# Kernel optimization log

Measured on AMD Instinct MI355X. Metric: run time of the kernel, lower is better.

The kernel has to match this reference:

```python
import jax, jax.numpy as jnp
import numpy as np

# Model dims (match init_kwargs)
NUM_INPUT_FEATURES = 100000
NUM_LABELS = 262144
EMBED_DIM = 256
H, DH = 4, 64          # num_heads, head_dim (EMBED_DIM = H*DH)
R, M = 2, 32           # num_quadrature_nodes, SLAY num_features
B, S = 4096, 64        # batch, history length
TOTAL_LABELS = 20480   # flattened ragged positive labels (~5/sample)
EPS = 1e-6
C = 2.0 + EPS

_nodes, _weights = np.polynomial.laguerre.laggauss(R)
QUAD_NODES = jnp.asarray(_nodes, dtype=jnp.float32) / C
QUAD_WEIGHTS = jnp.asarray(_weights, dtype=jnp.float32) / C


def slay_features(x, omega):
    """SLAY feature map. x: [N, EMBED_DIM] -> [N, H*R*M]."""
    n = x.shape[0]
    xr = x.reshape(n, H, DH)
    norm = jnp.linalg.norm(xr, axis=-1, keepdims=True)
    xn = xr / jnp.maximum(norm, 1e-6)                      # safe_normalize
    proj = jnp.einsum('bhd,rhdm->rbhm', xn, omega)         # [R,N,H,M]
    inv_sqrt_m = 1.0 / jnp.sqrt(jnp.float32(M))
    poly = (proj * proj) * inv_sqrt_m
    s = QUAD_NODES.reshape(-1, 1, 1, 1)
    sqrt_2s = jnp.sqrt(2.0 * jnp.maximum(s, 0.0))
    prf = jnp.exp(jnp.clip(proj * sqrt_2s - s, -10.0, 10.0)) * inv_sqrt_m
    w = jnp.sqrt(jnp.maximum(QUAD_WEIGHTS.reshape(-1, 1, 1, 1), 0.0))
    fused = poly * prf * w                                 # [R,N,H,M]
    return fused.transpose(1, 2, 0, 3).reshape(n, -1)      # [N, H*R*M]


def setup_inputs() -> dict:
    key = jax.random.key(0)
    k1, k2, k3, k4, k5 = jax.random.split(key, 5)
    indices = jax.random.randint(k1, (B, S), 0, NUM_INPUT_FEATURES, dtype=jnp.int64)
    mask = jnp.ones((B, S), dtype=jnp.float32)
    flat_labels = jax.random.randint(k2, (TOTAL_LABELS,), 0, NUM_LABELS, dtype=jnp.int64)
    sample_ids = jnp.sort(jax.random.randint(k3, (TOTAL_LABELS,), 0, B, dtype=jnp.int64))
    embed_table = jax.random.normal(k4, (NUM_INPUT_FEATURES, EMBED_DIM), dtype=jnp.float32)
    kw, ko = jax.random.split(k5)
    W_vecs = jax.random.normal(kw, (NUM_LABELS, EMBED_DIM), dtype=jnp.float32) / jnp.sqrt(jnp.float32(EMBED_DIM))
    omega = jax.random.normal(ko, (R, H, DH, M), dtype=jnp.float32)
    return {"indices": indices, "mask": mask, "flat_labels": flat_labels,
            "sample_ids": sample_ids, "embed_table": embed_table,
            "W_vecs": W_vecs, "omega": omega}


def reference(indices, mask, flat_labels, sample_ids, embed_table, W_vecs, omega):
    # MeanEmbedding encoder
    embeds = embed_table[indices]                                   # [B,S,D]
    sum_emb = jnp.sum(embeds * mask[:, :, None], axis=1)
    query = sum_emb / jnp.maximum(jnp.sum(mask, axis=1, keepdims=True), 1e-9)
    phi_q = slay_features(query, omega)                             # [B,F]
    phi_W = slay_features(W_vecs, omega)                            # [L,F]
    Z_vec = jnp.sum(phi_W, axis=0)                                  # [F]
    log_Z = jnp.log(phi_q @ Z_vec + 1e-6)                           # [B]
    # ragged positive-label terms, flattened (same math as per-sample loop)
    nums = jnp.sum(phi_W[flat_labels] * phi_q[sample_ids], axis=-1) + 1e-6
    loss_total = -jnp.sum(jnp.log(nums) - log_Z[sample_ids])
    return loss_total / B
```

## Files before the change

kernel.cpp:

```cpp
#include <hip/hip_runtime.h>
#include <hip/hip_bf16.h>
#include <math.h>

#define BB 4096
#define SS 64
#define DD 256
#define NH 4
#define DH 64
#define MM 32
#define NLAB 262144
#define TLAB 20480
#define ISM 0.17677669529663687f

typedef __attribute__((ext_vector_type(8))) short short8;
typedef __attribute__((ext_vector_type(4))) float f32x4;

static __device__ __forceinline__ short f2bf(float f) {
    __hip_bfloat16 h = __float2bfloat16(f);
    return *reinterpret_cast<short*>(&h);
}

__global__ __launch_bounds__(256) void k_query_phi(
    const int* __restrict__ idx, const float* __restrict__ mask,
    const float* __restrict__ emb, const float* __restrict__ omega,
    float* __restrict__ phiq, float* __restrict__ Zvec,
    float s0f, float s1f, float q0f, float q1f, float cw0, float cw1)
{
    const int b = blockIdx.x, t = threadIdx.x;
    const int h = t >> 6, r = (t >> 5) & 1, m = t & 31;
    if (b == 0) Zvec[t] = 0.0f;

    __shared__ int   lidx[SS];
    __shared__ float lmk[SS];
    if (t < SS) { lidx[t] = idx[b * SS + t]; lmk[t] = mask[b * SS + t]; }

    float omg[DH];
    const float* ob = omega + (size_t)((r * NH + h) * DH) * MM + m;
#pragma unroll
    for (int d = 0; d < DH; ++d) omg[d] = ob[d * MM];

    __syncthreads();

    float acc = 0.0f, msum = 0.0f;
#pragma unroll 8
    for (int s = 0; s < SS; ++s) {
        int   id = lidx[s];
        float mv = lmk[s];
        acc   = fmaf(emb[(size_t)id * DD + t], mv, acc);
        msum += mv;
    }
    float q = acc / fmaxf(msum, 1e-9f);

    float ss = q * q;
#pragma unroll
    for (int off = 32; off >= 1; off >>= 1) ss += __shfl_xor(ss, off);
    float xn = q / fmaxf(sqrtf(ss), 1e-6f);

    __shared__ float lxn[DD];
    lxn[t] = xn;
    __syncthreads();

    float p = 0.0f;
    const float* xb = lxn + h * DH;
#pragma unroll
    for (int d = 0; d < DH; ++d) p = fmaf(xb[d], omg[d], p);

    const float sv = r ? s1f : s0f, qv = r ? q1f : q0f, cw = r ? cw1 : cw0;
    float arg = fminf(fmaxf(fmaf(p, qv, -sv), -10.0f), 10.0f);
    phiq[b * DD + t] = p * p * __expf(arg) * cw;
}

__global__ __launch_bounds__(256) void k_zvec(
    const float* __restrict__ W, const float* __restrict__ omega,
    float* __restrict__ Zvec, int lab_per_block,
    float s0f, float s1f, float q0f, float q1f, float cw0, float cw1)
{
    const int t = threadIdx.x;
    const int h    = t >> 6;
    const int lane = t & 63;
    const int l15  = lane & 15;
    const int kg   = lane >> 4;

    short8 bf[4][2];
#pragma unroll
    for (int nt = 0; nt < 4; ++nt) {
        const int r = nt >> 1;
        const int m = (nt & 1) * 16 + l15;
        const float* ob = omega + (size_t)((r * NH + h) * DH) * MM + m;
#pragma unroll
        for (int kh = 0; kh < 2; ++kh)
#pragma unroll
            for (int e = 0; e < 8; ++e) {
                int d = kh * 32 + kg * 8 + e;
                bf[nt][kh][e] = f2bf(ob[(size_t)d * MM]);
            }
    }

    float zp[4] = {0.0f, 0.0f, 0.0f, 0.0f};
    const int l0 = blockIdx.x * lab_per_block;

    for (int tile = 0; tile < lab_per_block; tile += 16) {
        const float* wp = W + (size_t)(l0 + tile + l15) * DD + h * DH + kg * 8;
        float4 f0 = *(const float4*)(wp);
        float4 f1 = *(const float4*)(wp + 4);
        float4 f2 = *(const float4*)(wp + 32);
        float4 f3 = *(const float4*)(wp + 36);

        float ss = f0.x*f0.x + f0.y*f0.y + f0.z*f0.z + f0.w*f0.w
                 + f1.x*f1.x + f1.y*f1.y + f1.z*f1.z + f1.w*f1.w
                 + f2.x*f2.x + f2.y*f2.y + f2.z*f2.z + f2.w*f2.w
                 + f3.x*f3.x + f3.y*f3.y + f3.z*f3.z + f3.w*f3.w;
        ss += __shfl_xor(ss, 16);
        ss += __shfl_xor(ss, 32);
        float rn = 1.0f / fmaxf(sqrtf(ss), 1e-6f);

        float rnr[4];
#pragma unroll
        for (int rr = 0; rr < 4; ++rr) rnr[rr] = __shfl(rn, kg * 4 + rr);

        short8 a0, a1;
        a0[0]=f2bf(f0.x); a0[1]=f2bf(f0.y); a0[2]=f2bf(f0.z); a0[3]=f2bf(f0.w);
        a0[4]=f2bf(f1.x); a0[5]=f2bf(f1.y); a0[6]=f2bf(f1.z); a0[7]=f2bf(f1.w);
        a1[0]=f2bf(f2.x); a1[1]=f2bf(f2.y); a1[2]=f2bf(f2.z); a1[3]=f2bf(f2.w);
        a1[4]=f2bf(f3.x); a1[5]=f2bf(f3.y); a1[6]=f2bf(f3.z); a1[7]=f2bf(f3.w);

        f32x4 acc[4];
#pragma unroll
        for (int nt = 0; nt < 4; ++nt) {
            f32x4 c = {0.0f, 0.0f, 0.0f, 0.0f};
            c = __builtin_amdgcn_mfma_f32_16x16x32_bf16(a0, bf[nt][0], c, 0, 0, 0);
            c = __builtin_amdgcn_mfma_f32_16x16x32_bf16(a1, bf[nt][1], c, 0, 0, 0);
            acc[nt] = c;
        }

#pragma unroll
        for (int nt = 0; nt < 4; ++nt) {
            const float qv = (nt >> 1) ? q1f : q0f;
            const float sv = (nt >> 1) ? s1f : s0f;
            const float cw = (nt >> 1) ? cw1 : cw0;
            float zs = 0.0f;
#pragma unroll
            for (int rr = 0; rr < 4; ++rr) {
                float p   = acc[nt][rr] * rnr[rr];
                float arg = fminf(fmaxf(fmaf(p, qv, -sv), -10.0f), 10.0f);
                zs = fmaf(p * p * __expf(arg), cw, zs);
            }
            zp[nt] += zs;
        }
    }

#pragma unroll
    for (int nt = 0; nt < 4; ++nt) {
        float z = zp[nt];
        z += __shfl_xor(z, 16);
        z += __shfl_xor(z, 32);
        if (lane < 16) atomicAdd(&Zvec[h * 64 + nt * 16 + lane], z);
    }
}

__global__ __launch_bounds__(256) void k_logz(
    const float* __restrict__ phiq, const float* __restrict__ Zvec,
    float* __restrict__ logZ, float* __restrict__ out)
{
    const int t = threadIdx.x, w = t >> 6, lane = t & 63;
    if (blockIdx.x == 0 && t == 0) out[0] = 0.0f;
    const int row = blockIdx.x * 4 + w;
    const float4* p4 = (const float4*)(phiq + (size_t)row * DD);
    const float4* z4 = (const float4*)Zvec;
    float4 a = p4[lane], z = z4[lane];
    float dot = a.x * z.x + a.y * z.y + a.z * z.z + a.w * z.w;
#pragma unroll
    for (int off = 32; off >= 1; off >>= 1) dot += __shfl_xor(dot, off);
    if (lane == 0) logZ[row] = logf(dot + 1e-6f);
}

__global__ __launch_bounds__(256) void k_loss(
    const int* __restrict__ flab, const int* __restrict__ sids,
    const float* __restrict__ W, const float* __restrict__ omega,
    const float* __restrict__ phiq, const float* __restrict__ logZ,
    float* __restrict__ out, int lab_per_block,
    float s0f, float s1f, float q0f, float q1f, float cw0, float cw1)
{
    const int t = threadIdx.x;
    const int h = t >> 6, r = (t >> 5) & 1, m = t & 31;
    const int wid = t >> 6, lane = t & 63;

    float omg[DH];
    const float* ob = omega + (size_t)((r * NH + h) * DH) * MM + m;
#pragma unroll
    for (int d = 0; d < DH; ++d) omg[d] = ob[d * MM];

    const float sv = r ? s1f : s0f, qv = r ? q1f : q0f, cw = r ? cw1 : cw0;

    __shared__ float lxn[DD];
    __shared__ float wpart[4];
    float acc = 0.0f;
    const int i0 = blockIdx.x * lab_per_block;
    for (int i = 0; i < lab_per_block; ++i) {
        const int gi  = i0 + i;
        const int l   = flab[gi];
        const int sid = sids[gi];
        float x = W[(size_t)l * DD + t];
        float ss = x * x;
#pragma unroll
        for (int off = 32; off >= 1; off >>= 1) ss += __shfl_xor(ss, off);
        float xn = x / fmaxf(sqrtf(ss), 1e-6f);
        lxn[t] = xn;
        __syncthreads();
        float p = 0.0f;
        const float* xb = lxn + h * DH;
#pragma unroll
        for (int d = 0; d < DH; ++d) p = fmaf(xb[d], omg[d], p);
        float arg = fminf(fmaxf(fmaf(p, qv, -sv), -10.0f), 10.0f);
        float phi = p * p * __expf(arg) * cw;
        float prod = phi * phiq[(size_t)sid * DD + t];
#pragma unroll
        for (int off = 32; off >= 1; off >>= 1) prod += __shfl_xor(prod, off);
        if (lane == 0) wpart[wid] = prod;
        __syncthreads();
        if (t == 0) {
            float num = wpart[0] + wpart[1] + wpart[2] + wpart[3] + 1e-6f;
            acc += logZ[sid] - logf(num);
        }
    }
    if (t == 0) atomicAdd(out, acc * (1.0f / (float)BB));
}

extern "C" void kernel_launch(void* const* d_in, const int* in_sizes, int n_in,
                              void* d_out, int out_size, void* d_ws, size_t ws_size,
                              hipStream_t stream) {
    const int*   indices = (const int*)  d_in[0];
    const float* mask    = (const float*)d_in[1];
    const int*   flab    = (const int*)  d_in[2];
    const int*   sids    = (const int*)  d_in[3];
    const float* emb     = (const float*)d_in[4];
    const float* W       = (const float*)d_in[5];
    const float* omega   = (const float*)d_in[6];
    float* out = (float*)d_out;

    float* ws   = (float*)d_ws;
    float* phiq = ws;
    float* Zvec = phiq + BB * DD;
    float* logZ = Zvec + DD;

    const double C  = 2.0 + 1e-6;
    const double s2 = sqrt(2.0);
    const double n0 = (2.0 - s2) / C, n1 = (2.0 + s2) / C;
    const double wt0 = ((2.0 + s2) / 4.0) / C, wt1 = ((2.0 - s2) / 4.0) / C;
    const float s0f = (float)n0,        s1f = (float)n1;
    const float q0f = (float)sqrt(2.0 * n0), q1f = (float)sqrt(2.0 * n1);
    const float cw0 = (float)(ISM * ISM * sqrt(wt0));
    const float cw1 = (float)(ISM * ISM * sqrt(wt1));

    k_query_phi<<<BB, 256, 0, stream>>>(indices, mask, emb, omega, phiq, Zvec,
                                        s0f, s1f, q0f, q1f, cw0, cw1);
    const int LPB = 256;
    k_zvec<<<NLAB / LPB, 256, 0, stream>>>(W, omega, Zvec, LPB,
                                           s0f, s1f, q0f, q1f, cw0, cw1);
    k_logz<<<BB / 4, 256, 0, stream>>>(phiq, Zvec, logZ, out);
    const int LPB2 = 8;
    k_loss<<<TLAB / LPB2, 256, 0, stream>>>(flab, sids, W, omega, phiq, logZ,
                                            out, LPB2,
                                            s0f, s1f, q0f, q1f, cw0, cw1);
}
```

Baseline: 510.8 us.

## Split query gather from phi, reuse MFMA path for query and loss features

```diff
diff --git a/kernel.cpp b/kernel.cpp
--- a/kernel.cpp
+++ b/kernel.cpp
@@ -12,6 +12,9 @@
 #define TLAB 20480
 #define ISM 0.17677669529663687f
 
+#define NZBLK 1024
+#define NQBLK 16
+
 typedef __attribute__((ext_vector_type(8))) short short8;
 typedef __attribute__((ext_vector_type(4))) float f32x4;
 
@@ -20,66 +23,54 @@
     return *reinterpret_cast<short*>(&h);
 }
 
-__global__ __launch_bounds__(256) void k_query_phi(
+__global__ __launch_bounds__(256) void k_gather(
     const int* __restrict__ idx, const float* __restrict__ mask,
-    const float* __restrict__ emb, const float* __restrict__ omega,
-    float* __restrict__ phiq, float* __restrict__ Zvec,
-    float s0f, float s1f, float q0f, float q1f, float cw0, float cw1)
+    const float* __restrict__ emb, float* __restrict__ xq,
+    float* __restrict__ Zvec)
 {
-    const int b = blockIdx.x, t = threadIdx.x;
-    const int h = t >> 6, r = (t >> 5) & 1, m = t & 31;
-    if (b == 0) Zvec[t] = 0.0f;
-
-    __shared__ int   lidx[SS];
-    __shared__ float lmk[SS];
-    if (t < SS) { lidx[t] = idx[b * SS + t]; lmk[t] = mask[b * SS + t]; }
-
-    float omg[DH];
-    const float* ob = omega + (size_t)((r * NH + h) * DH) * MM + m;
-#pragma unroll
-    for (int d = 0; d < DH; ++d) omg[d] = ob[d * MM];
-
-    __syncthreads();
-
-    float acc = 0.0f, msum = 0.0f;
+    const int t = threadIdx.x, w = t >> 6, lane = t & 63;
+    const int b = blockIdx.x * 4 + w;
+    if (blockIdx.x == 0) Zvec[t] = 0.0f;
+
+    const int   id0 = idx [b * SS + lane];
+    const float mk0 = mask[b * SS + lane];
+    float msum = mk0;
+#pragma unroll
+    for (int off = 32; off >= 1; off >>= 1) msum += __shfl_xor(msum, off);
+
+    const float* ebase = emb + (size_t)lane * 4;
+    float4 acc = {0.f, 0.f, 0.f, 0.f};
 #pragma unroll 8
     for (int s = 0; s < SS; ++s) {
-        int   id = lidx[s];
-        float mv = lmk[s];
-        acc   = fmaf(emb[(size_t)id * DD + t], mv, acc);
-        msum += mv;
-    }
-    float q = acc / fmaxf(msum, 1e-9f);
-
-    float ss = q * q;
-#pragma unroll
-    for (int off = 32; off >= 1; off >>= 1) ss += __shfl_xor(ss, off);
-    float xn = q / fmaxf(sqrtf(ss), 1e-6f);
-
-    __shared__ float lxn[DD];
-    lxn[t] = xn;
-    __syncthreads();
-
-    float p = 0.0f;
-    const float* xb = lxn + h * DH;
-#pragma unroll
-    for (int d = 0; d < DH; ++d) p = fmaf(xb[d], omg[d], p);
-
-    const float sv = r ? s1f : s0f, qv = r ? q1f : q0f, cw = r ? cw1 : cw0;
-    float arg = fminf(fmaxf(fmaf(p, qv, -sv), -10.0f), 10.0f);
-    phiq[b * DD + t] = p * p * __expf(arg) * cw;
-}
-
-__global__ __launch_bounds__(256) void k_zvec(
-    const float* __restrict__ W, const float* __restrict__ omega,
-    float* __restrict__ Zvec, int lab_per_block,
+        const int   ids = __shfl(id0, s);
+        const float mv  = __shfl(mk0, s);
+        const float4 e = *(const float4*)(ebase + (size_t)ids * DD);
+        acc.x = fmaf(e.x, mv, acc.x);
+        acc.y = fmaf(e.y, mv, acc.y);
+        acc.z = fmaf(e.z, mv, acc.z);
+        acc.w = fmaf(e.w, mv, acc.w);
+    }
+    const float inv = 1.0f / fmaxf(msum, 1e-9f);
+    float4 q = {acc.x * inv, acc.y * inv, acc.z * inv, acc.w * inv};
+    float ss = q.x*q.x + q.y*q.y + q.z*q.z + q.w*q.w;
+    ss += __shfl_xor(ss, 1); ss += __shfl_xor(ss, 2);
+    ss += __shfl_xor(ss, 4); ss += __shfl_xor(ss, 8);
+    const float rn = 1.0f / fmaxf(sqrtf(ss), 1e-6f);
+    float4 xn = {q.x * rn, q.y * rn, q.z * rn, q.w * rn};
+    *(float4*)(xq + (size_t)b * DD + lane * 4) = xn;
+}
+
+__global__ __launch_bounds__(256) void k_phi(
+    const float* __restrict__ W, const float* __restrict__ xq,
+    const float* __restrict__ omega,
+    float* __restrict__ Zvec, float* __restrict__ phiq,
     float s0f, float s1f, float q0f, float q1f, float cw0, float cw1)
 {
     const int t = threadIdx.x;
-    const int h    = t >> 6;
-    const int lane = t & 63;
-    const int l15  = lane & 15;
-    const int kg   = lane >> 4;
+    const int h = t >> 6, lane = t & 63, l15 = lane & 15, kg = lane >> 4;
+    const bool isQ = blockIdx.x >= NZBLK;
+    const float* base = isQ ? xq : W;
+    const int l0 = (isQ ? (blockIdx.x - NZBLK) : blockIdx.x) * 256;
 
     short8 bf[4][2];
 #pragma unroll
@@ -90,44 +81,52 @@
 #pragma unroll
         for (int kh = 0; kh < 2; ++kh)
 #pragma unroll
-            for (int e = 0; e < 8; ++e) {
-                int d = kh * 32 + kg * 8 + e;
-                bf[nt][kh][e] = f2bf(ob[(size_t)d * MM]);
-            }
-    }
-
-    float zp[4] = {0.0f, 0.0f, 0.0f, 0.0f};
-    const int l0 = blockIdx.x * lab_per_block;
-
-    for (int tile = 0; tile < lab_per_block; tile += 16) {
-        const float* wp = W + (size_t)(l0 + tile + l15) * DD + h * DH + kg * 8;
-        float4 f0 = *(const float4*)(wp);
-        float4 f1 = *(const float4*)(wp + 4);
-        float4 f2 = *(const float4*)(wp + 32);
-        float4 f3 = *(const float4*)(wp + 36);
-
-        float ss = f0.x*f0.x + f0.y*f0.y + f0.z*f0.z + f0.w*f0.w
-                 + f1.x*f1.x + f1.y*f1.y + f1.z*f1.z + f1.w*f1.w
-                 + f2.x*f2.x + f2.y*f2.y + f2.z*f2.z + f2.w*f2.w
-                 + f3.x*f3.x + f3.y*f3.y + f3.z*f3.z + f3.w*f3.w;
-        ss += __shfl_xor(ss, 16);
-        ss += __shfl_xor(ss, 32);
-        float rn = 1.0f / fmaxf(sqrtf(ss), 1e-6f);
+            for (int e = 0; e < 8; ++e)
+                bf[nt][kh][e] = f2bf(ob[(size_t)(kh * 32 + kg * 8 + e) * MM]);
+    }
+
+    float zp[4] = {0.f, 0.f, 0.f, 0.f};
+    const float* sp = base + (size_t)(l0 + l15) * DD + h * DH + kg * 8;
+    float4 c0 = *(const float4*)(sp);
+    float4 c1 = *(const float4*)(sp + 4);
+    float4 c2 = *(const float4*)(sp + 32);
+    float4 c3 = *(const float4*)(sp + 36);
+
+    for (int tl = 0; tl < 16; ++tl) {
+        const float* np = sp + 16 * DD;
+        float4 n0 = c0, n1 = c1, n2 = c2, n3 = c3;
+        if (tl < 15) {
+            n0 = *(const float4*)(np);
+            n1 = *(const float4*)(np + 4);
+            n2 = *(const float4*)(np + 32);
+            n3 = *(const float4*)(np + 36);
+        }
 
         float rnr[4];
-#pragma unroll
-        for (int rr = 0; rr < 4; ++rr) rnr[rr] = __shfl(rn, kg * 4 + rr);
+        if (isQ) {
+            rnr[0] = rnr[1] = rnr[2] = rnr[3] = 1.0f;
+        } else {
+            float ss = c0.x*c0.x + c0.y*c0.y + c0.z*c0.z + c0.w*c0.w
+                     + c1.x*c1.x + c1.y*c1.y + c1.z*c1.z + c1.w*c1.w
+                     + c2.x*c2.x + c2.y*c2.y + c2.z*c2.z + c2.w*c2.w
+                     + c3.x*c3.x + c3.y*c3.y + c3.z*c3.z + c3.w*c3.w;
+            ss += __shfl_xor(ss, 16);
+            ss += __shfl_xor(ss, 32);
+            float rn = 1.0f / fmaxf(sqrtf(ss), 1e-6f);
+#pragma unroll
+            for (int rr = 0; rr < 4; ++rr) rnr[rr] = __shfl(rn, kg * 4 + rr);
+        }
 
         short8 a0, a1;
-        a0[0]=f2bf(f0.x); a0[1]=f2bf(f0.y); a0[2]=f2bf(f0.z); a0[3]=f2bf(f0.w);
-        a0[4]=f2bf(f1.x); a0[5]=f2bf(f1.y); a0[6]=f2bf(f1.z); a0[7]=f2bf(f1.w);
-        a1[0]=f2bf(f2.x); a1[1]=f2bf(f2.y); a1[2]=f2bf(f2.z); a1[3]=f2bf(f2.w);
-        a1[4]=f2bf(f3.x); a1[5]=f2bf(f3.y); a1[6]=f2bf(f3.z); a1[7]=f2bf(f3.w);
+        a0[0]=f2bf(c0.x); a0[1]=f2bf(c0.y); a0[2]=f2bf(c0.z); a0[3]=f2bf(c0.w);
+        a0[4]=f2bf(c1.x); a0[5]=f2bf(c1.y); a0[6]=f2bf(c1.z); a0[7]=f2bf(c1.w);
+        a1[0]=f2bf(c2.x); a1[1]=f2bf(c2.y); a1[2]=f2bf(c2.z); a1[3]=f2bf(c2.w);
+        a1[4]=f2bf(c3.x); a1[5]=f2bf(c3.y); a1[6]=f2bf(c3.z); a1[7]=f2bf(c3.w);
 
         f32x4 acc[4];
 #pragma unroll
         for (int nt = 0; nt < 4; ++nt) {
-            f32x4 c = {0.0f, 0.0f, 0.0f, 0.0f};
+            f32x4 c = {0.f, 0.f, 0.f, 0.f};
             c = __builtin_amdgcn_mfma_f32_16x16x32_bf16(a0, bf[nt][0], c, 0, 0, 0);
             c = __builtin_amdgcn_mfma_f32_16x16x32_bf16(a1, bf[nt][1], c, 0, 0, 0);
             acc[nt] = c;
@@ -143,18 +142,26 @@
             for (int rr = 0; rr < 4; ++rr) {
                 float p   = acc[nt][rr] * rnr[rr];
                 float arg = fminf(fmaxf(fmaf(p, qv, -sv), -10.0f), 10.0f);
-                zs = fmaf(p * p * __expf(arg), cw, zs);
+                float phi = p * p * __expf(arg) * cw;
+                if (isQ)
+                    phiq[(size_t)(l0 + tl * 16 + kg * 4 + rr) * DD
+                         + h * 64 + nt * 16 + l15] = phi;
+                else
+                    zs += phi;
             }
             zp[nt] += zs;
         }
-    }
-
-#pragma unroll
-    for (int nt = 0; nt < 4; ++nt) {
-        float z = zp[nt];
-        z += __shfl_xor(z, 16);
-        z += __shfl_xor(z, 32);
-        if (lane < 16) atomicAdd(&Zvec[h * 64 + nt * 16 + lane], z);
+        sp = np; c0 = n0; c1 = n1; c2 = n2; c3 = n3;
+    }
+
+    if (!isQ) {
+#pragma unroll
+        for (int nt = 0; nt < 4; ++nt) {
+            float z = zp[nt];
+            z += __shfl_xor(z, 16);
+            z += __shfl_xor(z, 32);
+            if (lane < 16) atomicAdd(&Zvec[h * 64 + nt * 16 + lane], z);
+        }
     }
 }
 
@@ -178,52 +185,102 @@
     const int* __restrict__ flab, const int* __restrict__ sids,
     const float* __restrict__ W, const float* __restrict__ omega,
     const float* __restrict__ phiq, const float* __restrict__ logZ,
-    float* __restrict__ out, int lab_per_block,
+    float* __restrict__ out,
     float s0f, float s1f, float q0f, float q1f, float cw0, float cw1)
 {
     const int t = threadIdx.x;
-    const int h = t >> 6, r = (t >> 5) & 1, m = t & 31;
-    const int wid = t >> 6, lane = t & 63;
-
-    float omg[DH];
-    const float* ob = omega + (size_t)((r * NH + h) * DH) * MM + m;
-#pragma unroll
-    for (int d = 0; d < DH; ++d) omg[d] = ob[d * MM];
-
-    const float sv = r ? s1f : s0f, qv = r ? q1f : q0f, cw = r ? cw1 : cw0;
-
-    __shared__ float lxn[DD];
-    __shared__ float wpart[4];
-    float acc = 0.0f;
-    const int i0 = blockIdx.x * lab_per_block;
-    for (int i = 0; i < lab_per_block; ++i) {
-        const int gi  = i0 + i;
-        const int l   = flab[gi];
-        const int sid = sids[gi];
-        float x = W[(size_t)l * DD + t];
-        float ss = x * x;
-#pragma unroll
-        for (int off = 32; off >= 1; off >>= 1) ss += __shfl_xor(ss, off);
-        float xn = x / fmaxf(sqrtf(ss), 1e-6f);
-        lxn[t] = xn;
-        __syncthreads();
-        float p = 0.0f;
-        const float* xb = lxn + h * DH;
-#pragma unroll
-        for (int d = 0; d < DH; ++d) p = fmaf(xb[d], omg[d], p);
-        float arg = fminf(fmaxf(fmaf(p, qv, -sv), -10.0f), 10.0f);
-        float phi = p * p * __expf(arg) * cw;
-        float prod = phi * phiq[(size_t)sid * DD + t];
-#pragma unroll
-        for (int off = 32; off >= 1; off >>= 1) prod += __shfl_xor(prod, off);
-        if (lane == 0) wpart[wid] = prod;
-        __syncthreads();
-        if (t == 0) {
-            float num = wpart[0] + wpart[1] + wpart[2] + wpart[3] + 1e-6f;
-            acc += logZ[sid] - logf(num);
-        }
-    }
-    if (t == 0) atomicAdd(out, acc * (1.0f / (float)BB));
+    const int h = t >> 6, lane = t & 63, l15 = lane & 15, kg = lane >> 4;
+    const int i0 = blockIdx.x * 16;
+
+    short8 bf[4][2];
+#pragma unroll
+    for (int nt = 0; nt < 4; ++nt) {
+        const int r = nt >> 1;
+        const int m = (nt & 1) * 16 + l15;
+        const float* ob = omega + (size_t)((r * NH + h) * DH) * MM + m;
+#pragma unroll
+        for (int kh = 0; kh < 2; ++kh)
+#pragma unroll
+            for (int e = 0; e < 8; ++e)
+                bf[nt][kh][e] = f2bf(ob[(size_t)(kh * 32 + kg * 8 + e) * MM]);
+    }
+
+    const int lab = flab[i0 + l15];
+    const int sid = sids[i0 + l15];
+    const float* wp = W + (size_t)lab * DD + h * DH + kg * 8;
+    float4 c0 = *(const float4*)(wp);
+    float4 c1 = *(const float4*)(wp + 4);
+    float4 c2 = *(const float4*)(wp + 32);
+    float4 c3 = *(const float4*)(wp + 36);
+
+    float ss = c0.x*c0.x + c0.y*c0.y + c0.z*c0.z + c0.w*c0.w
+             + c1.x*c1.x + c1.y*c1.y + c1.z*c1.z + c1.w*c1.w
+             + c2.x*c2.x + c2.y*c2.y + c2.z*c2.z + c2.w*c2.w
+             + c3.x*c3.x + c3.y*c3.y + c3.z*c3.z + c3.w*c3.w;
+    ss += __shfl_xor(ss, 16);
+    ss += __shfl_xor(ss, 32);
+    float rn = 1.0f / fmaxf(sqrtf(ss), 1e-6f);
+    float rnr[4];
+    int   sidr[4];
+#pragma unroll
+    for (int rr = 0; rr < 4; ++rr) {
+        rnr[rr]  = __shfl(rn,  kg * 4 + rr);
+        sidr[rr] = __shfl(sid, kg * 4 + rr);
+    }
+
+    short8 a0, a1;
+    a0[0]=f2bf(c0.x); a0[1]=f2bf(c0.y); a0[2]=f2bf(c0.z); a0[3]=f2bf(c0.w);
+    a0[4]=f2bf(c1.x); a0[5]=f2bf(c1.y); a0[6]=f2bf(c1.z); a0[7]=f2bf(c1.w);
+    a1[0]=f2bf(c2.x); a1[1]=f2bf(c2.y); a1[2]=f2bf(c2.z); a1[3]=f2bf(c2.w);
+    a1[4]=f2bf(c3.x); a1[5]=f2bf(c3.y); a1[6]=f2bf(c3.z); a1[7]=f2bf(c3.w);
+
+    f32x4 acc[4];
+#pragma unroll
+    for (int nt = 0; nt < 4; ++nt) {
+        f32x4 c = {0.f, 0.f, 0.f, 0.f};
+        c = __builtin_amdgcn_mfma_f32_16x16x32_bf16(a0, bf[nt][0], c, 0, 0, 0);
+        c = __builtin_amdgcn_mfma_f32_16x16x32_bf16(a1, bf[nt][1], c, 0, 0, 0);
+        acc[nt] = c;
+    }
+
+    float part[4] = {0.f, 0.f, 0.f, 0.f};
+#pragma unroll
+    for (int nt = 0; nt < 4; ++nt) {
+        const float qv = (nt >> 1) ? q1f : q0f;
+        const float sv = (nt >> 1) ? s1f : s0f;
+        const float cw = (nt >> 1) ? cw1 : cw0;
+#pragma unroll
+        for (int rr = 0; rr < 4; ++rr) {
+            float p   = acc[nt][rr] * rnr[rr];
+            float arg = fminf(fmaxf(fmaf(p, qv, -sv), -10.0f), 10.0f);
+            float phi = p * p * __expf(arg) * cw;
+            part[rr] = fmaf(phi,
+                            phiq[(size_t)sidr[rr] * DD + h * 64 + nt * 16 + l15],
+                            part[rr]);
+        }
+    }
+#pragma unroll
+    for (int rr = 0; rr < 4; ++rr) {
+        part[rr] += __shfl_xor(part[rr], 1);
+        part[rr] += __shfl_xor(part[rr], 2);
+        part[rr] += __shfl_xor(part[rr], 4);
+        part[rr] += __shfl_xor(part[rr], 8);
+    }
+    __shared__ float lsum[NH][16];
+    if (l15 == 0) {
+#pragma unroll
+        for (int rr = 0; rr < 4; ++rr) lsum[h][kg * 4 + rr] = part[rr];
+    }
+    __syncthreads();
+    if (t < 16) {
+        float num = lsum[0][t] + lsum[1][t] + lsum[2][t] + lsum[3][t] + 1e-6f;
+        float term = logZ[sids[i0 + t]] - logf(num);
+        term += __shfl_xor(term, 1);
+        term += __shfl_xor(term, 2);
+        term += __shfl_xor(term, 4);
+        term += __shfl_xor(term, 8);
+        if (t == 0) atomicAdd(out, term * (1.0f / (float)BB));
+    }
 }
 
 extern "C" void kernel_launch(void* const* d_in, const int* in_sizes, int n_in,
@@ -242,6 +299,7 @@
     float* phiq = ws;
     float* Zvec = phiq + BB * DD;
     float* logZ = Zvec + DD;
+    float* xq   = logZ + BB;
 
     const double C  = 2.0 + 1e-6;
     const double s2 = sqrt(2.0);
@@ -252,14 +310,10 @@
     const float cw0 = (float)(ISM * ISM * sqrt(wt0));
     const float cw1 = (float)(ISM * ISM * sqrt(wt1));
 
-    k_query_phi<<<BB, 256, 0, stream>>>(indices, mask, emb, omega, phiq, Zvec,
-                                        s0f, s1f, q0f, q1f, cw0, cw1);
-    const int LPB = 256;
-    k_zvec<<<NLAB / LPB, 256, 0, stream>>>(W, omega, Zvec, LPB,
-                                           s0f, s1f, q0f, q1f, cw0, cw1);
+    k_gather<<<BB / 4, 256, 0, stream>>>(indices, mask, emb, xq, Zvec);
+    k_phi<<<NZBLK + NQBLK, 256, 0, stream>>>(W, xq, omega, Zvec, phiq,
+                                             s0f, s1f, q0f, q1f, cw0, cw1);
     k_logz<<<BB / 4, 256, 0, stream>>>(phiq, Zvec, logZ, out);
-    const int LPB2 = 8;
-    k_loss<<<TLAB / LPB2, 256, 0, stream>>>(flab, sids, W, omega, phiq, logZ,
-                                            out, LPB2,
-                                            s0f, s1f, q0f, q1f, cw0, cw1);
-}
+    k_loss<<<TLAB / 16, 256, 0, stream>>>(flab, sids, W, omega, phiq, logZ,
+                                          out, s0f, s1f, q0f, q1f, cw0, cw1);
+}
```

Measured after the change: 483.8 us. 5.3% less time.
